# Optimization experiments

Measured on AMD Instinct MI355X. Metric: run time of the kernel, lower is better.

Reference implementation:

```python
import jax, jax.numpy as jnp
import numpy as np

N = 50000      # nodes
E = 800000     # edges (avg degree 16)
D = 64         # embedding_dim
G = 64         # graphs in batch
V = 30         # node label vocab (hard-coded in module)


def setup_inputs() -> dict:
    key = jax.random.key(0)
    ks = jax.random.split(key, 12)
    x = jax.random.randint(ks[0], (N,), 0, V, dtype=jnp.int32)
    edge_index = jax.random.randint(ks[1], (2, E), 0, N, dtype=jnp.int32)
    edge_attr = jax.random.uniform(ks[2], (E,), dtype=jnp.float32)
    batch = jnp.sort(jax.random.randint(ks[3], (N,), 0, G, dtype=jnp.int32))
    emb = jax.random.normal(ks[4], (V, D), dtype=jnp.float32)
    s = 1.0 / np.sqrt(D)
    W1 = jax.random.uniform(ks[5], (D, D), jnp.float32, -s, s)
    b1 = jnp.zeros((D,), jnp.float32)
    W2 = jax.random.uniform(ks[6], (D, D), jnp.float32, -s, s)
    b2 = jnp.zeros((D,), jnp.float32)
    W3 = jax.random.uniform(ks[7], (D, D), jnp.float32, -s, s)
    b3 = jnp.zeros((D,), jnp.float32)
    return {"x": x, "edge_index": edge_index, "edge_attr": edge_attr,
            "batch": batch, "emb": emb, "W1": W1, "b1": b1,
            "W2": W2, "b2": b2, "W3": W3, "b3": b3}


def _gcn(h, W, b, src, dst, norm, inv_deg):
    # GCNConv with self-loops: out_i = sum_{j->i} norm_ij * (h_j W) + (1/deg_i) * (h_i W) + b
    h = h @ W
    agg = jax.ops.segment_sum(h[src] * norm[:, None], dst, num_segments=N)
    return agg + h * inv_deg[:, None] + b


def reference(x, edge_index, edge_attr, batch, emb, W1, b1, W2, b2, W3, b3):
    src, dst = edge_index[0], edge_index[1]
    # symmetric GCN normalization with self-loops (weight 1)
    deg = jax.ops.segment_sum(edge_attr, dst, num_segments=N) + 1.0
    dis = deg ** -0.5                      # deg >= 1, so finite
    norm = dis[src] * edge_attr * dis[dst]
    inv_deg = 1.0 / deg                    # self-loop norm = dis_i * 1 * dis_i

    h = emb[x]                             # [N, D]
    h = jax.nn.relu(_gcn(h, W1, b1, src, dst, norm, inv_deg))
    h = jax.nn.relu(_gcn(h, W2, b2, src, dst, norm, inv_deg))
    h = _gcn(h, W3, b3, src, dst, norm, inv_deg)

    # global_mean_pool over graph ids
    sums = jax.ops.segment_sum(h, batch, num_segments=G)          # [G, D]
    cnts = jax.ops.segment_sum(jnp.ones((N,), h.dtype), batch, num_segments=G)
    pooled = sums / jnp.maximum(cnts, 1.0)[:, None]
    # L2 normalize rows
    nrm = jnp.linalg.norm(pooled, axis=1, keepdims=True)
    return pooled / jnp.maximum(nrm, 1e-12)
```

## Files before the change

### kernel.cpp

```cpp
#include <hip/hip_runtime.h>
#include <hip/hip_fp16.h>
#include <hip/hip_fp8.h>

#define NN 50000
#define NE 800000
#define DD 64
#define GG 64
#define VV 30
#define CAP 48
#define PBLK 512
#define PCH ((NN + PBLK - 1) / PBLK)
#define BINW 128
#define NBIN ((NN + BINW - 1) / BINW)
#define NCH 256
#define CHE ((NE + NCH - 1) / NCH)
#define SLOT 2560

__device__ inline unsigned char f2fp8(float f) {
    __hip_fp8_e4m3 t(f);
    return *reinterpret_cast<unsigned char*>(&t);
}
__device__ inline float fp82f(unsigned char c) {
    __hip_fp8_e4m3 t;
    *reinterpret_cast<unsigned char*>(&t) = c;
    return (float)t;
}
__device__ inline unsigned pack_edge(int s, float ea) {
    return (unsigned)s | ((unsigned)__half_as_ushort(__float2half_rn(ea)) << 16);
}
__device__ inline int unpack_src(unsigned p) { return (int)(p & 0xFFFFu); }
__device__ inline float unpack_ea(unsigned p) {
    return __half2float(__ushort_as_half((unsigned short)(p >> 16)));
}

__global__ __launch_bounds__(256) void k_hist(const int* __restrict__ dst,
                                              int* __restrict__ hist,
                                              const float* __restrict__ emb,
                                              const float* __restrict__ W1,
                                              float* __restrict__ E1,
                                              float* __restrict__ pool,
                                              float* __restrict__ gcnt) {
    __shared__ int lh[NBIN];
    int t = threadIdx.x, ch = blockIdx.x;
    if (ch == 0) {
        for (int i = t; i < VV * DD; i += 256) {
            int vv = i >> 6, d = i & 63;
            float acc = 0.f;
            #pragma unroll
            for (int k = 0; k < 64; k++) acc = fmaf(emb[vv * 64 + k], W1[k * 64 + d], acc);
            E1[i] = acc;
        }
    } else if (ch == 1) {
        for (int i = t; i < GG * DD; i += 256) pool[i] = 0.f;
        if (t < GG) gcnt[t] = 0.f;
    }
    for (int b = t; b < NBIN; b += 256) lh[b] = 0;
    __syncthreads();
    int e0 = ch * CHE, e1 = min(e0 + CHE, NE);
    for (int e = e0 + t; e < e1; e += 256) atomicAdd(&lh[dst[e] >> 7], 1);
    __syncthreads();
    for (int b = t; b < NBIN; b += 256) hist[ch * NBIN + b] = lh[b];
}

__global__ __launch_bounds__(NCH) void k_scan_chunks(int* __restrict__ hist,
                                                     int* __restrict__ totals) {
    __shared__ int ts[NCH];
    int t = threadIdx.x, b = blockIdx.x;
    int v = hist[t * NBIN + b];
    ts[t] = v;
    __syncthreads();
    for (int off = 1; off < NCH; off <<= 1) {
        int u = (t >= off) ? ts[t - off] : 0;
        __syncthreads();
        ts[t] += u;
        __syncthreads();
    }
    hist[t * NBIN + b] = ts[t] - v;
    if (t == NCH - 1) totals[b] = ts[t];
}

__global__ __launch_bounds__(256) void k_scatter_bins(const int* __restrict__ src,
                                                      const int* __restrict__ dst,
                                                      const float* __restrict__ ea,
                                                      const int* __restrict__ hist,
                                                      uint2* __restrict__ sem) {
    __shared__ int lbase[NBIN];
    int t = threadIdx.x, ch = blockIdx.x;
    for (int b = t; b < NBIN; b += 256)
        lbase[b] = b * SLOT + hist[ch * NBIN + b];
    __syncthreads();
    int e0 = ch * CHE, e1 = min(e0 + CHE, NE);
    for (int e = e0 + t; e < e1; e += 256) {
        int d = dst[e];
        int bin = d >> 7;
        int p = atomicAdd(&lbase[bin], 1);
        if (p < (bin + 1) * SLOT)
            sem[p] = make_uint2(pack_edge(src[e], ea[e]), (unsigned)(d & (BINW - 1)));
    }
}

__global__ __launch_bounds__(256) void k_build(const int* __restrict__ totals,
                                               const uint2* __restrict__ sem,
                                               unsigned* __restrict__ ep,
                                               int* __restrict__ cnt,
                                               float* __restrict__ dis) {
    __shared__ int   lcnt[BINW];
    __shared__ float lsum[BINW];
    int t = threadIdx.x, b = blockIdx.x;
    if (t < BINW) { lcnt[t] = 0; lsum[t] = 0.f; }
    __syncthreads();
    int e0 = b * SLOT, e1 = e0 + min(totals[b], SLOT);
    for (int e = e0 + t; e < e1; e += 256) {
        uint2 u = sem[e];
        int local = (int)u.y;
        int p = atomicAdd(&lcnt[local], 1);
        if (p < CAP) ep[(size_t)(b * BINW + local) * CAP + p] = u.x;
        atomicAdd(&lsum[local], unpack_ea(u.x));
    }
    __syncthreads();
    if (t < BINW) {
        int node = b * BINW + t;
        if (node < NN) {
            cnt[node] = lcnt[t];
            dis[node] = 1.0f / sqrtf(1.0f + lsum[t]);
        }
    }
}

__global__ __launch_bounds__(256) void k_layer1mm(const int* __restrict__ cnt,
                                                  const unsigned* __restrict__ ep,
                                                  const float* __restrict__ dis,
                                                  const int* __restrict__ x,
                                                  const float* __restrict__ E1,
                                                  const float* __restrict__ b1,
                                                  const float* __restrict__ W2,
                                                  unsigned char* __restrict__ B) {
    __shared__ float El[VV * 64];
    __shared__ float Wl[64 * 64];
    __shared__ float hl[4 * 64];
    int t = threadIdx.x;
    for (int i = t; i < VV * 64; i += 256) El[i] = E1[i];
    for (int i = t * 4; i < 64 * 64; i += 256 * 4)
        *(float4*)&Wl[i] = *(const float4*)&W2[i];
    __syncthreads();
    int wave = t >> 6, d = t & 63;
    int node = blockIdx.x * 4 + wave;
    int c = min(cnt[node], CAP);
    const unsigned* row = ep + (size_t)node * CAP;
    unsigned pay = (d < c) ? row[d] : 0u;
    float disn = dis[node];
    float a0 = 0.f, a1 = 0.f, a2 = 0.f, a3 = 0.f;
    int iters = (c + 7) >> 3;
    for (int it = 0; it < iters; ++it) {
        int k0 = it << 3;
        unsigned p0 = __shfl(pay, k0+0), p1 = __shfl(pay, k0+1);
        unsigned p2 = __shfl(pay, k0+2), p3 = __shfl(pay, k0+3);
        unsigned p4 = __shfl(pay, k0+4), p5 = __shfl(pay, k0+5);
        unsigned p6 = __shfl(pay, k0+6), p7 = __shfl(pay, k0+7);
        int s0 = unpack_src(p0), s1 = unpack_src(p1), s2 = unpack_src(p2), s3 = unpack_src(p3);
        int s4 = unpack_src(p4), s5 = unpack_src(p5), s6 = unpack_src(p6), s7 = unpack_src(p7);
        int x0 = x[s0], x1 = x[s1], x2 = x[s2], x3 = x[s3];
        int x4 = x[s4], x5 = x[s5], x6 = x[s6], x7 = x[s7];
        float w0 = dis[s0] * unpack_ea(p0), w1 = dis[s1] * unpack_ea(p1);
        float w2 = dis[s2] * unpack_ea(p2), w3 = dis[s3] * unpack_ea(p3);
        float w4 = dis[s4] * unpack_ea(p4), w5 = dis[s5] * unpack_ea(p5);
        float w6 = dis[s6] * unpack_ea(p6), w7 = dis[s7] * unpack_ea(p7);
        a0 = fmaf(w0, El[x0 * 64 + d], a0); a1 = fmaf(w1, El[x1 * 64 + d], a1);
        a2 = fmaf(w2, El[x2 * 64 + d], a2); a3 = fmaf(w3, El[x3 * 64 + d], a3);
        a0 = fmaf(w4, El[x4 * 64 + d], a0); a1 = fmaf(w5, El[x5 * 64 + d], a1);
        a2 = fmaf(w6, El[x6 * 64 + d], a2); a3 = fmaf(w7, El[x7 * 64 + d], a3);
    }
    float v = ((a0 + a1) + (a2 + a3)) * disn
            + El[x[node] * 64 + d] * (disn * disn) + b1[d];
    hl[wave * 64 + d] = fmaxf(v, 0.f);
    __syncthreads();
    float acc = 0.f;
    #pragma unroll
    for (int k = 0; k < 64; k++) acc = fmaf(hl[wave * 64 + k], Wl[k * 64 + d], acc);
    if (node < NN) B[(size_t)node * 64 + d] = f2fp8(acc);
}

__global__ __launch_bounds__(256) void k_spmm2(const int* __restrict__ cnt,
                                               const unsigned* __restrict__ ep,
                                               const float* __restrict__ dis,
                                               const unsigned char* __restrict__ B,
                                               const float* __restrict__ bias,
                                               unsigned char* __restrict__ A2) {
    int node = blockIdx.x * 4 + (threadIdx.x >> 6);
    int d = threadIdx.x & 63;
    if (node >= NN) return;
    int c = min(cnt[node], CAP);
    const unsigned* row = ep + (size_t)node * CAP;
    unsigned pay = (d < c) ? row[d] : 0u;
    float disn = dis[node];
    float a0 = 0.f, a1 = 0.f, a2 = 0.f, a3 = 0.f;
    int iters = (c + 7) >> 3;
    for (int it = 0; it < iters; ++it) {
        int k0 = it << 3;
        unsigned p0 = __shfl(pay, k0+0), p1 = __shfl(pay, k0+1);
        unsigned p2 = __shfl(pay, k0+2), p3 = __shfl(pay, k0+3);
        unsigned p4 = __shfl(pay, k0+4), p5 = __shfl(pay, k0+5);
        unsigned p6 = __shfl(pay, k0+6), p7 = __shfl(pay, k0+7);
        int s0 = unpack_src(p0), s1 = unpack_src(p1), s2 = unpack_src(p2), s3 = unpack_src(p3);
        int s4 = unpack_src(p4), s5 = unpack_src(p5), s6 = unpack_src(p6), s7 = unpack_src(p7);
        float g0 = fp82f(B[(size_t)s0 * 64 + d]), g1 = fp82f(B[(size_t)s1 * 64 + d]);
        float g2 = fp82f(B[(size_t)s2 * 64 + d]), g3 = fp82f(B[(size_t)s3 * 64 + d]);
        float g4 = fp82f(B[(size_t)s4 * 64 + d]), g5 = fp82f(B[(size_t)s5 * 64 + d]);
        float g6 = fp82f(B[(size_t)s6 * 64 + d]), g7 = fp82f(B[(size_t)s7 * 64 + d]);
        float w0 = dis[s0] * unpack_ea(p0), w1 = dis[s1] * unpack_ea(p1);
        float w2 = dis[s2] * unpack_ea(p2), w3 = dis[s3] * unpack_ea(p3);
        float w4 = dis[s4] * unpack_ea(p4), w5 = dis[s5] * unpack_ea(p5);
        float w6 = dis[s6] * unpack_ea(p6), w7 = dis[s7] * unpack_ea(p7);
        a0 = fmaf(w0, g0, a0); a1 = fmaf(w1, g1, a1);
        a2 = fmaf(w2, g2, a2); a3 = fmaf(w3, g3, a3);
        a0 = fmaf(w4, g4, a0); a1 = fmaf(w5, g5, a1);
        a2 = fmaf(w6, g6, a2); a3 = fmaf(w7, g7, a3);
    }
    float v = ((a0 + a1) + (a2 + a3)) * disn
            + fp82f(B[(size_t)node * 64 + d]) * (disn * disn) + bias[d];
    A2[(size_t)node * 64 + d] = f2fp8(fmaxf(v, 0.f));
}

__global__ __launch_bounds__(1024) void k_spmm3_pool(const int* __restrict__ cnt,
                                                     const unsigned* __restrict__ ep,
                                                     const float* __restrict__ dis,
                                                     const unsigned char* __restrict__ A2,
                                                     const int* __restrict__ batch,
                                                     float* __restrict__ pool,
                                                     float* __restrict__ gcnt) {
    __shared__ float lpool[GG * DD];
    __shared__ float lcnt[GG];
    int t = threadIdx.x;
    for (int i = t; i < GG * DD; i += 1024) lpool[i] = 0.f;
    if (t < GG) lcnt[t] = 0.f;
    __syncthreads();
    int base = blockIdx.x * PCH;
    int end = min(base + PCH, NN);
    int d = t & 63;
    int curg = -1;
    float racc = 0.f, rcnt = 0.f;
    for (int node = base + (t >> 6); node < end; node += 16) {
        int c = min(cnt[node], CAP);
        const unsigned* row = ep + (size_t)node * CAP;
        unsigned pay = (d < c) ? row[d] : 0u;
        float disn = dis[node];
        float a0 = 0.f, a1 = 0.f, a2 = 0.f, a3 = 0.f;
        int iters = (c + 7) >> 3;
        for (int it = 0; it < iters; ++it) {
            int k0 = it << 3;
            unsigned p0 = __shfl(pay, k0+0), p1 = __shfl(pay, k0+1);
            unsigned p2 = __shfl(pay, k0+2), p3 = __shfl(pay, k0+3);
            unsigned p4 = __shfl(pay, k0+4), p5 = __shfl(pay, k0+5);
            unsigned p6 = __shfl(pay, k0+6), p7 = __shfl(pay, k0+7);
            int s0 = unpack_src(p0), s1 = unpack_src(p1), s2 = unpack_src(p2), s3 = unpack_src(p3);
            int s4 = unpack_src(p4), s5 = unpack_src(p5), s6 = unpack_src(p6), s7 = unpack_src(p7);
            float g0 = fp82f(A2[(size_t)s0 * 64 + d]), g1 = fp82f(A2[(size_t)s1 * 64 + d]);
            float g2 = fp82f(A2[(size_t)s2 * 64 + d]), g3 = fp82f(A2[(size_t)s3 * 64 + d]);
            float g4 = fp82f(A2[(size_t)s4 * 64 + d]), g5 = fp82f(A2[(size_t)s5 * 64 + d]);
            float g6 = fp82f(A2[(size_t)s6 * 64 + d]), g7 = fp82f(A2[(size_t)s7 * 64 + d]);
            float w0 = dis[s0] * unpack_ea(p0), w1 = dis[s1] * unpack_ea(p1);
            float w2 = dis[s2] * unpack_ea(p2), w3 = dis[s3] * unpack_ea(p3);
            float w4 = dis[s4] * unpack_ea(p4), w5 = dis[s5] * unpack_ea(p5);
            float w6 = dis[s6] * unpack_ea(p6), w7 = dis[s7] * unpack_ea(p7);
            a0 = fmaf(w0, g0, a0); a1 = fmaf(w1, g1, a1);
            a2 = fmaf(w2, g2, a2); a3 = fmaf(w3, g3, a3);
            a0 = fmaf(w4, g4, a0); a1 = fmaf(w5, g5, a1);
            a2 = fmaf(w6, g6, a2); a3 = fmaf(w7, g7, a3);
        }
        float v = ((a0 + a1) + (a2 + a3)) * disn
                + fp82f(A2[(size_t)node * 64 + d]) * (disn * disn);
        int g = batch[node];
        if (g != curg) {
            if (curg >= 0) {
                atomicAdd(&lpool[curg * 64 + d], racc);
                if (d == 0) atomicAdd(&lcnt[curg], rcnt);
            }
            curg = g; racc = 0.f; rcnt = 0.f;
        }
        racc += v; rcnt += 1.f;
    }
    if (curg >= 0) {
        atomicAdd(&lpool[curg * 64 + d], racc);
        if (d == 0) atomicAdd(&lcnt[curg], rcnt);
    }
    __syncthreads();
    for (int i = t; i < GG * DD; i += 1024) {
        float v = lpool[i];
        if (v != 0.f) unsafeAtomicAdd(&pool[i], v);
    }
    if (t < GG) {
        float v = lcnt[t];
        if (v != 0.f) unsafeAtomicAdd(&gcnt[t], v);
    }
}

__global__ __launch_bounds__(1024) void k_final_mm(const float* __restrict__ pool,
                                                   const float* __restrict__ gcnt,
                                                   const float* __restrict__ W3,
                                                   const float* __restrict__ b3,
                                                   float* __restrict__ out) {
    __shared__ float Wl[DD * DD];
    __shared__ float Ml[GG * DD];
    int t = threadIdx.x;
    for (int i = t; i < DD * DD; i += 1024) Wl[i] = W3[i];
    for (int i = t; i < GG * DD; i += 1024) {
        int g = i >> 6;
        Ml[i] = pool[i] / fmaxf(gcnt[g], 1.0f);
    }
    __syncthreads();
    int w = t >> 6, d = t & 63;
    for (int g = w; g < GG; g += 16) {
        float acc = b3[d];
        #pragma unroll
        for (int k = 0; k < 64; k++) acc = fmaf(Ml[g * 64 + k], Wl[k * 64 + d], acc);
        float ss = acc * acc;
        #pragma unroll
        for (int o = 32; o > 0; o >>= 1) ss += __shfl_xor(ss, o);
        out[g * 64 + d] = acc / fmaxf(sqrtf(ss), 1e-12f);
    }
}

extern "C" void kernel_launch(void* const* d_in, const int* in_sizes, int n_in,
                              void* d_out, int out_size, void* d_ws, size_t ws_size,
                              hipStream_t stream) {
    const int*   x    = (const int*)d_in[0];
    const int*   ei   = (const int*)d_in[1];
    const int*   src  = ei;
    const int*   dst  = ei + NE;
    const float* ea   = (const float*)d_in[2];
    const int*   batch= (const int*)d_in[3];
    const float* emb  = (const float*)d_in[4];
    const float* W1 = (const float*)d_in[5],  *b1 = (const float*)d_in[6];
    const float* W2 = (const float*)d_in[7],  *b2 = (const float*)d_in[8];
    const float* W3 = (const float*)d_in[9],  *b3 = (const float*)d_in[10];
    float* out = (float*)d_out;

    char* ws = (char*)d_ws;
    size_t off = 0;
    auto alloc = [&](size_t nb) -> void* {
        void* p = ws + off;
        off = (off + nb + 255) & ~(size_t)255;
        return p;
    };
    float*          dis    = (float*)alloc((size_t)NN * 4);
    int*            cntN   = (int*)  alloc((size_t)NN * 4);
    unsigned*       ep     = (unsigned*)alloc((size_t)NBIN * BINW * CAP * 4);
    int*            hist   = (int*)  alloc((size_t)NCH * NBIN * 4);
    int*            totals = (int*)  alloc((size_t)NBIN * 4);
    uint2*          sem    = (uint2*)alloc((size_t)NBIN * SLOT * 8);
    unsigned char*  B      = (unsigned char*)alloc((size_t)NN * DD);
    unsigned char*  A2     = (unsigned char*)alloc((size_t)NN * DD);
    float*          E1     = (float*)alloc((size_t)VV * DD * 4);
    float*          pool   = (float*)alloc((size_t)GG * DD * 4);
    float*          gcnt   = (float*)alloc((size_t)GG * 4);

    k_hist<<<NCH, 256, 0, stream>>>(dst, hist, emb, W1, E1, pool, gcnt);
    k_scan_chunks<<<NBIN, NCH, 0, stream>>>(hist, totals);
    k_scatter_bins<<<NCH, 256, 0, stream>>>(src, dst, ea, hist, sem);
    k_build<<<NBIN, 256, 0, stream>>>(totals, sem, ep, cntN, dis);

    k_layer1mm<<<NN / 4, 256, 0, stream>>>(cntN, ep, dis, x, E1, b1, W2, B);

    k_spmm2<<<(NN + 3) / 4, 256, 0, stream>>>(cntN, ep, dis, B, b2, A2);

    k_spmm3_pool<<<PBLK, 1024, 0, stream>>>(cntN, ep, dis, A2, batch, pool, gcnt);

    k_final_mm<<<1, 1024, 0, stream>>>(pool, gcnt, W3, b3, out);
}
```

Measured before the change: 147.6 us.

## Split layer-1 aggregation from W2 matmul into separate bf16-staged kernel

The fused layer-1 kernel, which did both sparse aggregation and the dense 64x64 W2 multiply per block of 4 nodes, is split in two. The aggregation kernel now writes ReLU outputs as bf16 to a new buffer. A separate tiled matmul kernel loads W2 into shared memory once per 64 rows and writes fp8 output. This removes the per-block 16KB W2 load and the extra sync from the gather kernel, which should improve occupancy. In exchange it adds a kernel launch, an extra global round trip of 6.4MB, and bf16 rounding of the intermediate.

```diff
diff --git a/kernel.cpp b/kernel.cpp
--- a/kernel.cpp
+++ b/kernel.cpp
@@ -31,6 +31,13 @@
 __device__ inline int unpack_src(unsigned p) { return (int)(p & 0xFFFFu); }
 __device__ inline float unpack_ea(unsigned p) {
     return __half2float(__ushort_as_half((unsigned short)(p >> 16)));
+}
+__device__ inline unsigned short f2bf(float f) {
+    unsigned u = __float_as_uint(f);
+    return (unsigned short)((u + 0x7FFF + ((u >> 16) & 1)) >> 16);
+}
+__device__ inline float bf2f(unsigned short s) {
+    return __uint_as_float(((unsigned)s) << 16);
 }
 
 __global__ __launch_bounds__(256) void k_hist(const int* __restrict__ dst,
@@ -127,24 +134,20 @@
     }
 }
 
-__global__ __launch_bounds__(256) void k_layer1mm(const int* __restrict__ cnt,
-                                                  const unsigned* __restrict__ ep,
-                                                  const float* __restrict__ dis,
-                                                  const int* __restrict__ x,
-                                                  const float* __restrict__ E1,
-                                                  const float* __restrict__ b1,
-                                                  const float* __restrict__ W2,
-                                                  unsigned char* __restrict__ B) {
+__global__ __launch_bounds__(256) void k_layer1(const int* __restrict__ cnt,
+                                                const unsigned* __restrict__ ep,
+                                                const float* __restrict__ dis,
+                                                const int* __restrict__ x,
+                                                const float* __restrict__ E1,
+                                                const float* __restrict__ b1,
+                                                unsigned short* __restrict__ A1) {
     __shared__ float El[VV * 64];
-    __shared__ float Wl[64 * 64];
-    __shared__ float hl[4 * 64];
     int t = threadIdx.x;
     for (int i = t; i < VV * 64; i += 256) El[i] = E1[i];
-    for (int i = t * 4; i < 64 * 64; i += 256 * 4)
-        *(float4*)&Wl[i] = *(const float4*)&W2[i];
-    __syncthreads();
-    int wave = t >> 6, d = t & 63;
-    int node = blockIdx.x * 4 + wave;
+    __syncthreads();
+    int node = blockIdx.x * 4 + (t >> 6);
+    int d = t & 63;
+    if (node >= NN) return;
     int c = min(cnt[node], CAP);
     const unsigned* row = ep + (size_t)node * CAP;
     unsigned pay = (d < c) ? row[d] : 0u;
@@ -172,12 +175,52 @@
     }
     float v = ((a0 + a1) + (a2 + a3)) * disn
             + El[x[node] * 64 + d] * (disn * disn) + b1[d];
-    hl[wave * 64 + d] = fmaxf(v, 0.f);
-    __syncthreads();
-    float acc = 0.f;
-    #pragma unroll
-    for (int k = 0; k < 64; k++) acc = fmaf(hl[wave * 64 + k], Wl[k * 64 + d], acc);
-    if (node < NN) B[(size_t)node * 64 + d] = f2fp8(acc);
+    A1[(size_t)node * 64 + d] = f2bf(fmaxf(v, 0.f));
+}
+
+__global__ __launch_bounds__(256) void k_matmul(const unsigned short* __restrict__ A,
+                                                const float* __restrict__ W,
+                                                unsigned char* __restrict__ B) {
+    __shared__ float Wl[64 * 64];
+    __shared__ float Ar[16 * 64];
+    int t = threadIdx.x;
+    for (int i = t * 4; i < 64 * 64; i += 256 * 4)
+        *(float4*)&Wl[i] = *(const float4*)&W[i];
+    int q   = t & 15;
+    int sub = t >> 4;
+    int r0 = blockIdx.x * 64;
+    for (int rg = 0; rg < 64; rg += 16) {
+        __syncthreads();
+        {
+            int idx = t * 4;
+            int rr = idx >> 6, kk = idx & 63;
+            int r = r0 + rg + rr;
+            float4 a = make_float4(0.f, 0.f, 0.f, 0.f);
+            if (r < NN) {
+                ushort4 u = *(const ushort4*)&A[(size_t)r * DD + kk];
+                a = make_float4(bf2f(u.x), bf2f(u.y), bf2f(u.z), bf2f(u.w));
+            }
+            *(float4*)&Ar[idx] = a;
+        }
+        __syncthreads();
+        int r = r0 + rg + sub;
+        if (r < NN) {
+            float4 acc = make_float4(0.f, 0.f, 0.f, 0.f);
+            #pragma unroll
+            for (int k = 0; k < 64; k++) {
+                float a = Ar[sub * 64 + k];
+                float4 w4 = *(float4*)&Wl[k * 64 + q * 4];
+                acc.x = fmaf(a, w4.x, acc.x);
+                acc.y = fmaf(a, w4.y, acc.y);
+                acc.z = fmaf(a, w4.z, acc.z);
+                acc.w = fmaf(a, w4.w, acc.w);
+            }
+            uchar4 o;
+            o.x = f2fp8(acc.x); o.y = f2fp8(acc.y);
+            o.z = f2fp8(acc.z); o.w = f2fp8(acc.w);
+            *(uchar4*)&B[(size_t)r * DD + q * 4] = o;
+        }
+    }
 }
 
 __global__ __launch_bounds__(256) void k_spmm2(const int* __restrict__ cnt,
@@ -348,6 +391,7 @@
     int*            hist   = (int*)  alloc((size_t)NCH * NBIN * 4);
     int*            totals = (int*)  alloc((size_t)NBIN * 4);
     uint2*          sem    = (uint2*)alloc((size_t)NBIN * SLOT * 8);
+    unsigned short* A1     = (unsigned short*)alloc((size_t)NN * DD * 2);
     unsigned char*  B      = (unsigned char*)alloc((size_t)NN * DD);
     unsigned char*  A2     = (unsigned char*)alloc((size_t)NN * DD);
     float*          E1     = (float*)alloc((size_t)VV * DD * 4);
@@ -359,8 +403,9 @@
     k_scatter_bins<<<NCH, 256, 0, stream>>>(src, dst, ea, hist, sem);
     k_build<<<NBIN, 256, 0, stream>>>(totals, sem, ep, cntN, dis);
 
-    k_layer1mm<<<NN / 4, 256, 0, stream>>>(cntN, ep, dis, x, E1, b1, W2, B);
-
+    k_layer1<<<(NN + 3) / 4, 256, 0, stream>>>(cntN, ep, dis, x, E1, b1, A1);
+
+    k_matmul<<<(NN + 63) / 64, 256, 0, stream>>>(A1, W2, B);
     k_spmm2<<<(NN + 3) / 4, 256, 0, stream>>>(cntN, ep, dis, B, b2, A2);
 
     k_spmm3_pool<<<PBLK, 1024, 0, stream>>>(cntN, ep, dis, A2, batch, pool, gcnt);
```

Result: faster. 141.0 us (-4.4%).
